# Kernel optimization log

Hardware: AMD Instinct MI355X
Metric: run time of the kernel (lower is better)

## Reference

```python
import jax, jax.numpy as jnp
import numpy as np

B, N, K, DEG = 512, 128, 8, 16
NR = 200            # num_rels (padding idx = NR)
INP, SEM, EMB, L = 32, 16, 32, 3
FEAT = INP - SEM
NN = B * N
E = NN * DEG
OUT = L * EMB       # 96


def _gru_cell(x, h, Wih, Whh, bih, bhh):
    gi = x @ Wih.T + bih
    gh = h @ Whh.T + bhh
    ir, iz, i_n = jnp.split(gi, 3, axis=-1)
    hr, hz, hn = jnp.split(gh, 3, axis=-1)
    r = jax.nn.sigmoid(ir + hr)
    z = jax.nn.sigmoid(iz + hz)
    n = jnp.tanh(i_n + r * hn)
    return (1.0 - z) * n + z * h


def _run_gru(xs, h0, Wih, Whh, bih, bhh):
    # xs: [T, batch, in]
    def step(h, x):
        h2 = _gru_cell(x, h, Wih, Whh, bih, bhh)
        return h2, h2
    hT, ys = jax.lax.scan(step, h0, xs)
    return ys, hT


def _forward(feat, out_nei_rels, in_nei_rels, r_label_node, src, dst, etype, rel_labels,
             rel_emb, w_rel2ent_W, w_rel2ent_b, W_msg, W_self, b_gnn, W_rel,
             gru_bias, gru_Wih_f, gru_Whh_f, gru_bih_f, gru_bhh_f,
             gru_Wih_b, gru_Whh_b, gru_bih_b, gru_bhh_b,
             Wo_W, Wo_b, path_Wih, path_Whh, path_bih, path_bhh, fc_W, fc_b):
    # --- init_ent_emb_matrix: neighbor-relation attention vs target relation ---
    out_e = rel_emb[out_nei_rels]                      # [NN,K,INP]
    in_e = rel_emb[in_nei_rels]                        # [NN,K,INP]
    tgt = rel_emb[r_label_node]                        # [NN,INP]
    out_att = jax.nn.softmax(jnp.einsum('nkd,nd->nk', out_e, tgt), axis=1)
    in_att = jax.nn.softmax(jnp.einsum('nkd,nd->nk', in_e, tgt), axis=1)
    out_sem = jnp.einsum('nk,nkd->nd', out_att, out_e)
    in_sem = jnp.einsum('nk,nkd->nd', in_att, in_e)
    sem = jax.nn.sigmoid(jnp.concatenate([out_sem, in_sem], axis=1) @ w_rel2ent_W + w_rel2ent_b)
    h = jnp.concatenate([feat, sem], axis=1)           # [NN,INP]

    # --- RGCN-style relational message passing; repr = concat of layer outputs ---
    r = rel_emb
    deg = jnp.maximum(jax.ops.segment_sum(jnp.ones((E,), h.dtype), dst, NN), 1.0)[:, None]
    reprs = []
    for l in range(L):
        msg = h[src] * r[etype]                        # [E,EMB]  (gather-heavy)
        agg = jax.ops.segment_sum(msg, dst, NN) / deg  # mean aggregation
        h = jax.nn.relu(agg @ W_msg[l] + h @ W_self[l] + b_gnn[l])
        r = r @ W_rel[l]                               # relation stream (padding row stays 0)
        reprs.append(h)
    repr_ = jnp.concatenate(reprs, axis=1)             # [NN,OUT]
    r_emb_out = r                                      # [NR+1,EMB]

    # --- BatchGRU: bidirectional GRU over each graph's node sequence ---
    node = repr_.reshape(B, N, OUT)
    message = jax.nn.relu(node + gru_bias)
    h0 = jnp.max(node, axis=1)                         # per-graph max init hidden
    xs = jnp.swapaxes(message, 0, 1)                   # [N,B,OUT]
    ys_f, _ = _run_gru(xs, h0, gru_Wih_f, gru_Whh_f, gru_bih_f, gru_bhh_f)
    ys_b, _ = _run_gru(xs[::-1], h0, gru_Wih_b, gru_Whh_b, gru_bih_b, gru_bhh_b)
    gru_out = jnp.concatenate([ys_f, ys_b[::-1]], axis=-1)  # [N,B,2*OUT]
    repr2 = jax.nn.relu(jnp.swapaxes(gru_out, 0, 1).reshape(NN, 2 * OUT))
    node_hidden = jax.nn.relu(repr2 @ Wo_W + Wo_b)     # [NN,OUT]

    nh = node_hidden.reshape(B, N, OUT)
    g_out = jnp.mean(nh, axis=1)                       # mean_nodes
    head_embs = nh[:, 0]                               # node id==1 is node 0 of each graph
    tail_embs = nh[:, 1]                               # node id==2 is node 1 of each graph

    # --- nei_rel_path: GRU over (h_r, r_t, t_r) triples, attention aggregation ---
    in_rels = in_nei_rels.reshape(B, N, K)
    heads_rels = in_rels[:, 0]                         # [B,K]
    tails_rels = in_rels[:, 1]                         # [B,K]
    P = K * K
    paths = jnp.stack([
        jnp.repeat(heads_rels, K, axis=1),
        jnp.broadcast_to(rel_labels[:, None], (B, P)),
        jnp.tile(tails_rels, (1, K)),
    ], axis=-1).reshape(B * P, 3)
    pe = r_emb_out[paths]                              # [B*P,3,EMB]
    _, last = _run_gru(jnp.swapaxes(pe, 0, 1), jnp.zeros((B * P, EMB), pe.dtype),
                       path_Wih, path_Whh, path_bih, path_bhh)
    last = last.reshape(B, P, EMB)
    r_lab_e = r_emb_out[rel_labels]                    # [B,EMB]
    atts = jax.nn.softmax(jnp.einsum('bpe,be->bp', last, r_lab_e), axis=1)
    g_p = jnp.einsum('bp,bpe->be', atts, last)         # [B,EMB]

    g_rep = jnp.concatenate([g_out, head_embs, tail_embs, r_lab_e, g_p], axis=1)  # [B,352]
    return g_rep @ fc_W + fc_b                         # [B,1]


def setup_inputs():
    key = jax.random.key(0)
    ks = jax.random.split(key, 40)
    idx = iter(range(40))
    def nk():
        return ks[next(idx)]
    def _p(shape, scale=0.1):
        return jax.random.normal(nk(), shape, jnp.float32) * scale

    feat = jax.random.normal(nk(), (NN, FEAT), jnp.float32)
    out_nei_rels = jax.random.randint(nk(), (NN, K), 0, NR)
    in_nei_rels = jax.random.randint(nk(), (NN, K), 0, NR)
    rel_labels = jax.random.randint(nk(), (B,), 0, NR)
    r_label_node = jnp.repeat(rel_labels, N)
    gid = jnp.arange(E) // (N * DEG)                   # edges stay within their graph
    src = gid * N + jax.random.randint(nk(), (E,), 0, N)
    dst = gid * N + jax.random.randint(nk(), (E,), 0, N)
    etype = jax.random.randint(nk(), (E,), 0, NR)
    rel_emb = jax.random.normal(nk(), (NR + 1, INP), jnp.float32) * 0.5
    rel_emb = rel_emb.at[NR].set(0.0)                  # padding_idx row

    return {
        'feat': feat, 'out_nei_rels': out_nei_rels, 'in_nei_rels': in_nei_rels,
        'r_label_node': r_label_node, 'src': src, 'dst': dst, 'etype': etype,
        'rel_labels': rel_labels, 'rel_emb': rel_emb,
        'w_rel2ent_W': _p((2 * INP, SEM)), 'w_rel2ent_b': _p((SEM,)),
        'W_msg': _p((L, EMB, EMB)), 'W_self': _p((L, EMB, EMB)),
        'b_gnn': _p((L, EMB)), 'W_rel': _p((L, INP, INP)),
        'gru_bias': _p((OUT,)),
        'gru_Wih_f': _p((3 * OUT, OUT)), 'gru_Whh_f': _p((3 * OUT, OUT)),
        'gru_bih_f': _p((3 * OUT,)), 'gru_bhh_f': _p((3 * OUT,)),
        'gru_Wih_b': _p((3 * OUT, OUT)), 'gru_Whh_b': _p((3 * OUT, OUT)),
        'gru_bih_b': _p((3 * OUT,)), 'gru_bhh_b': _p((3 * OUT,)),
        'Wo_W': _p((2 * OUT, OUT)), 'Wo_b': _p((OUT,)),
        'path_Wih': _p((3 * EMB, EMB)), 'path_Whh': _p((3 * EMB, EMB)),
        'path_bih': _p((3 * EMB,)), 'path_bhh': _p((3 * EMB,)),
        'fc_W': _p((3 * OUT + 2 * EMB, 1)), 'fc_b': _p((1,)),
    }


def reference(feat, out_nei_rels, in_nei_rels, r_label_node, src, dst, etype, rel_labels,
              rel_emb, w_rel2ent_W, w_rel2ent_b, W_msg, W_self, b_gnn, W_rel,
              gru_bias, gru_Wih_f, gru_Whh_f, gru_bih_f, gru_bhh_f,
              gru_Wih_b, gru_Whh_b, gru_bih_b, gru_bhh_b,
              Wo_W, Wo_b, path_Wih, path_Whh, path_bih, path_bhh, fc_W, fc_b):
    return _forward(feat, out_nei_rels, in_nei_rels, r_label_node, src, dst, etype, rel_labels,
                    rel_emb, w_rel2ent_W, w_rel2ent_b, W_msg, W_self, b_gnn, W_rel,
                    gru_bias, gru_Wih_f, gru_Whh_f, gru_bih_f, gru_bhh_f,
                    gru_Wih_b, gru_Whh_b, gru_bih_b, gru_bhh_b,
                    Wo_W, Wo_b, path_Wih, path_Whh, path_bih, path_bhh, fc_W, fc_b)
```

## Files before the change

kernel.cpp:

```cpp
#include <hip/hip_runtime.h>
#include <math.h>

#define BB 512
#define NT 128
#define NREL 201
#define NNODE (BB*NT)
#define NEDGE (NNODE*16)

typedef float f32x4 __attribute__((ext_vector_type(4)));

__device__ __forceinline__ float sigm(float x) { return 1.f/(1.f + __expf(-x)); }

__global__ __launch_bounds__(96) void k_rel2(const float* __restrict__ rel_emb,
                                             const float* __restrict__ W_rel,
                                             const float* __restrict__ pWih,
                                             const float* __restrict__ pbih,
                                             float* __restrict__ r123,
                                             float* __restrict__ XI) {
  __shared__ float ra[32], rb[32];
  int r = blockIdx.x, tid = threadIdx.x;
  if (tid < 32) ra[tid] = rel_emb[r*32 + tid];
  __syncthreads();
  if (tid < 32) {
    float s = 0.f;
    #pragma unroll
    for (int d = 0; d < 32; ++d) s += ra[d]*W_rel[d*32 + tid];
    rb[tid] = s; r123[0*NREL*32 + r*32 + tid] = s;
  }
  __syncthreads();
  if (tid < 32) {
    float s = 0.f;
    #pragma unroll
    for (int d = 0; d < 32; ++d) s += rb[d]*W_rel[1024 + d*32 + tid];
    ra[tid] = s; r123[1*NREL*32 + r*32 + tid] = s;
  }
  __syncthreads();
  if (tid < 32) {
    float s = 0.f;
    #pragma unroll
    for (int d = 0; d < 32; ++d) s += ra[d]*W_rel[2048 + d*32 + tid];
    rb[tid] = s; r123[2*NREL*32 + r*32 + tid] = s;
  }
  __syncthreads();
  float s = pbih[tid];
  #pragma unroll
  for (int d = 0; d < 32; ++d) s += rb[d]*pWih[tid*32 + d];
  XI[r*96 + tid] = s;
}

__global__ __launch_bounds__(256) void k_wt1(const float* __restrict__ Wih_f,
                                             const float* __restrict__ Wih_b,
                                             const float* __restrict__ bih_f,
                                             const float* __restrict__ bih_b,
                                             float* __restrict__ WT1,
                                             float* __restrict__ bcat) {
  int i = blockIdx.x*256 + threadIdx.x;
  if (i < 96*576) {
    int k = i / 576, j = i - k*576;
    WT1[i] = (j < 288) ? Wih_f[j*96 + k] : Wih_b[(j-288)*96 + k];
  }
  if (i < 576) bcat[i] = (i < 288) ? bih_f[i] : bih_b[i-288];
}

__device__ __forceinline__ void sem_att(const float* __restrict__ rel_emb,
                                        const int rels[8], const float tgt[32],
                                        float out[32]) {
  float dots[8]; float mx = -1e30f;
  #pragma unroll
  for (int k = 0; k < 8; ++k) {
    const float4* er = (const float4*)(rel_emb + rels[k]*32);
    float s = 0.f;
    #pragma unroll
    for (int q = 0; q < 8; ++q) {
      float4 v = er[q];
      s += v.x*tgt[4*q+0] + v.y*tgt[4*q+1] + v.z*tgt[4*q+2] + v.w*tgt[4*q+3];
    }
    dots[k] = s; mx = fmaxf(mx, s);
  }
  float den = 0.f;
  #pragma unroll
  for (int k = 0; k < 8; ++k) { float e = __expf(dots[k]-mx); dots[k] = e; den += e; }
  float inv = 1.f/den;
  #pragma unroll
  for (int d = 0; d < 32; ++d) out[d] = 0.f;
  #pragma unroll
  for (int k = 0; k < 8; ++k) {
    const float4* er = (const float4*)(rel_emb + rels[k]*32);
    float a = dots[k]*inv;
    #pragma unroll
    for (int q = 0; q < 8; ++q) {
      float4 v = er[q];
      out[4*q+0] += a*v.x; out[4*q+1] += a*v.y; out[4*q+2] += a*v.z; out[4*q+3] += a*v.w;
    }
  }
}

__global__ __launch_bounds__(256) void k_sem(
    const float* __restrict__ feat, const int* __restrict__ out_rels,
    const int* __restrict__ in_rels, const int* __restrict__ r_label_node,
    const float* __restrict__ rel_emb, const float* __restrict__ W,
    const float* __restrict__ bias, float* __restrict__ hin) {
  int n = blockIdx.x*256 + threadIdx.x;
  float tgt[32];
  {
    const float4* tr = (const float4*)(rel_emb + r_label_node[n]*32);
    #pragma unroll
    for (int q = 0; q < 8; ++q) {
      float4 v = tr[q];
      tgt[4*q+0]=v.x; tgt[4*q+1]=v.y; tgt[4*q+2]=v.z; tgt[4*q+3]=v.w;
    }
  }
  int ro[8], ri[8];
  #pragma unroll
  for (int k = 0; k < 8; ++k) { ro[k] = out_rels[n*8+k]; ri[k] = in_rels[n*8+k]; }
  float osem[32], isem[32];
  sem_att(rel_emb, ro, tgt, osem);
  sem_att(rel_emb, ri, tgt, isem);
  const float4* fr = (const float4*)(feat + (size_t)n*16);
  float4* ho = (float4*)(hin + (size_t)n*32);
  #pragma unroll
  for (int q = 0; q < 4; ++q) ho[q] = fr[q];
  #pragma unroll
  for (int j = 0; j < 16; ++j) {
    float s = bias[j];
    #pragma unroll
    for (int d = 0; d < 32; ++d) s += osem[d]*W[d*16+j] + isem[d]*W[(32+d)*16+j];
    hin[(size_t)n*32 + 16 + j] = sigm(s);
  }
}

__global__ __launch_bounds__(512) void k_gnn3(
    const float* __restrict__ hin, const float* __restrict__ rel_emb,
    const float* __restrict__ r123,
    const int* __restrict__ src, const int* __restrict__ dst, const int* __restrict__ etype,
    const float* __restrict__ W_msg, const float* __restrict__ W_self,
    const float* __restrict__ b_gnn,
    float* __restrict__ AT, float* __restrict__ ghid0) {
  __shared__ __align__(16) float hl[NT*36];
  __shared__ __align__(16) float hnew[NT*33];
  __shared__ float rl[NREL*32];
  __shared__ unsigned short eidx[2048];
  __shared__ float scratch[16][32];
  __shared__ int cnt[128], fill[128], scanv[128], rowstart[129];
  int g = blockIdx.x;
  int tid = threadIdx.x;
  int d = tid & 31, grp = tid >> 5;

  for (int i = tid; i < NT*32; i += 512) {
    int row = i >> 5, col = i & 31;
    hl[row*36 + col] = hin[(size_t)(g*NT + row)*32 + col];
  }
  if (tid < 128) { cnt[tid] = 0; fill[tid] = 0; }
  __syncthreads();
  for (int i = tid; i < 2048; i += 512)
    atomicAdd(&cnt[dst[g*2048 + i] - g*NT], 1);
  __syncthreads();
  if (tid < 128) scanv[tid] = cnt[tid];
  __syncthreads();
  #pragma unroll
  for (int off = 1; off < 128; off <<= 1) {
    int v = 0;
    if (tid < 128 && tid >= off) v = scanv[tid - off];
    __syncthreads();
    if (tid < 128) scanv[tid] += v;
    __syncthreads();
  }
  if (tid < 128) { rowstart[tid+1] = scanv[tid]; if (tid == 0) rowstart[0] = 0; }
  __syncthreads();
  for (int i = tid; i < 2048; i += 512) {
    int e = g*2048 + i;
    int dl = dst[e] - g*NT;
    int slot = rowstart[dl] + atomicAdd(&fill[dl], 1);
    eidx[slot] = (unsigned short)(((src[e] - g*NT) << 8) | etype[e]);
  }

  for (int l = 0; l < 3; ++l) {
    const float* rsrc = (l == 0) ? rel_emb : (r123 + (size_t)(l-1)*NREL*32);
    for (int i = tid; i < NREL*32; i += 512) rl[i] = rsrc[i];
    float wm[32], ws[32];
    #pragma unroll
    for (int dd = 0; dd < 32; ++dd) {
      wm[dd] = W_msg[l*1024 + dd*32 + d];
      ws[dd] = W_self[l*1024 + dd*32 + d];
    }
    float bj = b_gnn[l*32 + d];
    __syncthreads();
    for (int k2 = 0; k2 < 8; ++k2) {
      int n = grp + k2*16;
      int e0 = rowstart[n], e1 = rowstart[n+1];
      float acc = 0.f;
      for (int e = e0; e < e1; ++e) {
        int pk = eidx[e];
        acc += hl[(pk >> 8)*36 + d] * rl[(pk & 255)*32 + d];
      }
      scratch[grp][d] = acc;
      float invd = 1.f / (float)((e1 - e0) > 0 ? (e1 - e0) : 1);
      float sa = 0.f, sh = 0.f;
      #pragma unroll
      for (int dd = 0; dd < 32; ++dd) {
        sa += scratch[grp][dd]*wm[dd];
        sh += hl[n*36 + dd]*ws[dd];
      }
      hnew[n*33 + d] = fmaxf(bj + invd*sa + sh, 0.f);
    }
    __syncthreads();
    for (int i = tid; i < NT*32; i += 512) {
      int row = i >> 5, col = i & 31;
      hl[row*36 + col] = hnew[row*33 + col];
    }
    #pragma unroll
    for (int pass = 0; pass < 8; ++pass) {
      int col = (pass << 2) + (tid >> 7);
      int row = tid & 127;
      AT[(size_t)(l*32 + col)*NNODE + g*NT + row] = hnew[row*33 + col];
    }
    {
      float m = -1e30f;
      #pragma unroll
      for (int k2 = 0; k2 < 8; ++k2) m = fmaxf(m, hnew[(grp + k2*16)*33 + d]);
      scratch[grp][d] = m;
    }
    __syncthreads();
    if (tid < 32) {
      float m = -1e30f;
      #pragma unroll
      for (int p2 = 0; p2 < 16; ++p2) m = fmaxf(m, scratch[p2][tid]);
      ghid0[g*96 + l*32 + tid] = m;
    }
    __syncthreads();
  }
}

__global__ __launch_bounds__(256) void k_gemm1(
    const float* __restrict__ AT, const float* __restrict__ gbias,
    const float* __restrict__ WT1, const float* __restrict__ bcat,
    float* __restrict__ GI) {
  __shared__ __align__(16) float As[96*128];
  __shared__ __align__(16) float Bs[96*64];
  int mb = blockIdx.x;
  int m0 = mb*128;
  int tid = threadIdx.x;
  for (int i = tid; i < 3072; i += 256) {
    int r = i >> 5, c4 = i & 31;
    float4 v = *(const float4*)&AT[(size_t)r*NNODE + m0 + c4*4];
    float b = gbias[r];
    float4 o = make_float4(fmaxf(v.x+b,0.f), fmaxf(v.y+b,0.f), fmaxf(v.z+b,0.f), fmaxf(v.w+b,0.f));
    *(float4*)&As[r*128 + c4*4] = o;
  }
  int tc = tid & 15, tr = tid >> 4;
  int r0 = tr*8, c0 = tc*4;
  for (int nb = 0; nb < 9; ++nb) {
    int n0 = nb*64;
    for (int i = tid; i < 1536; i += 256) {
      int r = i >> 4, c4 = i & 15;
      *(float4*)&Bs[r*64 + c4*4] = *(const float4*)&WT1[r*576 + n0 + c4*4];
    }
    __syncthreads();
    float acc[8][4] = {};
    #pragma unroll 4
    for (int k = 0; k < 96; ++k) {
      float4 a0 = *(float4*)&As[k*128 + r0];
      float4 a1 = *(float4*)&As[k*128 + r0 + 4];
      float4 b  = *(float4*)&Bs[k*64 + c0];
      acc[0][0]+=a0.x*b.x; acc[0][1]+=a0.x*b.y; acc[0][2]+=a0.x*b.z; acc[0][3]+=a0.x*b.w;
      acc[1][0]+=a0.y*b.x; acc[1][1]+=a0.y*b.y; acc[1][2]+=a0.y*b.z; acc[1][3]+=a0.y*b.w;
      acc[2][0]+=a0.z*b.x; acc[2][1]+=a0.z*b.y; acc[2][2]+=a0.z*b.z; acc[2][3]+=a0.z*b.w;
      acc[3][0]+=a0.w*b.x; acc[3][1]+=a0.w*b.y; acc[3][2]+=a0.w*b.z; acc[3][3]+=a0.w*b.w;
      acc[4][0]+=a1.x*b.x; acc[4][1]+=a1.x*b.y; acc[4][2]+=a1.x*b.z; acc[4][3]+=a1.x*b.w;
      acc[5][0]+=a1.y*b.x; acc[5][1]+=a1.y*b.y; acc[5][2]+=a1.y*b.z; acc[5][3]+=a1.y*b.w;
      acc[6][0]+=a1.z*b.x; acc[6][1]+=a1.z*b.y; acc[6][2]+=a1.z*b.z; acc[6][3]+=a1.z*b.w;
      acc[7][0]+=a1.w*b.x; acc[7][1]+=a1.w*b.y; acc[7][2]+=a1.w*b.z; acc[7][3]+=a1.w*b.w;
    }
    float4 bia = *(const float4*)&bcat[n0 + c0];
    #pragma unroll
    for (int r = 0; r < 8; ++r) {
      f32x4 o = { acc[r][0]+bia.x, acc[r][1]+bia.y, acc[r][2]+bia.z, acc[r][3]+bia.w };
      __builtin_nontemporal_store(o, (f32x4*)&GI[(size_t)(m0 + r0 + r)*576 + n0 + c0]);
    }
    __syncthreads();
  }
}

#define PIN4(v) asm volatile("" : "+v"(v.x), "+v"(v.y), "+v"(v.z), "+v"(v.w))
#define DOT16(acc, W0,W1,W2,W3, X0,X1,X2,X3) \
  acc += W0.x*X0.x + W0.y*X0.y + W0.z*X0.z + W0.w*X0.w \
       + W1.x*X1.x + W1.y*X1.y + W1.z*X1.z + W1.w*X1.w \
       + W2.x*X2.x + W2.y*X2.y + W2.z*X2.z + W2.w*X2.w \
       + W3.x*X3.x + W3.y*X3.y + W3.z*X3.z + W3.w*X3.w

__global__ __launch_bounds__(576, 1) void k_gru(
    const float* __restrict__ Whh_f, const float* __restrict__ bhh_f,
    const float* __restrict__ Whh_b, const float* __restrict__ bhh_b,
    const float* __restrict__ GI, const float* __restrict__ ghid0,
    float* __restrict__ AT2) {
  __shared__ __align__(16) float h_lds[4][96];
  __shared__ float part[4][288][9];
  int bx = blockIdx.x;
  int dir = bx >> 7;
  int gbase = (bx & 127) * 4;
  int tid = threadIdx.x;
  int c = tid % 96;
  int p = tid / 96;
  bool fin = (tid < 384);
  int s = p;

  const float* Whh = dir ? Whh_b : Whh_f;
  const float4* wr0 = (const float4*)(Whh + (size_t)c*96 + p*16);
  const float4* wr1 = (const float4*)(Whh + (size_t)(96+c)*96 + p*16);
  const float4* wr2 = (const float4*)(Whh + (size_t)(192+c)*96 + p*16);
  float4 wa0=wr0[0], wa1=wr0[1], wa2=wr0[2], wa3=wr0[3];
  float4 wb0=wr1[0], wb1=wr1[1], wb2=wr1[2], wb3=wr1[3];
  float4 wc0=wr2[0], wc1=wr2[1], wc2=wr2[2], wc3=wr2[3];

  float bh0=0.f, bh1=0.f, bh2=0.f;
  float gi0=0.f, gi1=0.f, gi2=0.f;
  if (fin) {
    const float* bhh = dir ? bhh_b : bhh_f;
    bh0 = bhh[c]; bh1 = bhh[96+c]; bh2 = bhh[192+c];
    h_lds[s][c] = ghid0[(gbase+s)*96 + c];
    int pos0 = dir ? 127 : 0;
    const float* g = GI + (size_t)((gbase+s)*128 + pos0)*576 + dir*288;
    gi0 = g[c]; gi1 = g[96+c]; gi2 = g[192+c];
  }
  __syncthreads();
  for (int t = 0; t < 128; ++t) {
    PIN4(wa0); PIN4(wa1); PIN4(wa2); PIN4(wa3);
    PIN4(wb0); PIN4(wb1); PIN4(wb2); PIN4(wb3);
    PIN4(wc0); PIN4(wc1); PIN4(wc2); PIN4(wc3);
    int pos = dir ? (127-t) : t;
    float gn0=0.f, gn1=0.f, gn2=0.f;
    if (fin && t < 127) {
      int posn = dir ? (126-t) : (t+1);
      const float* g = GI + (size_t)((gbase+s)*128 + posn)*576 + dir*288;
      gn0 = g[c]; gn1 = g[96+c]; gn2 = g[192+c];
    }
    #pragma unroll
    for (int s4 = 0; s4 < 4; ++s4) {
      const float4* hh = (const float4*)&h_lds[s4][p*16];
      float4 x0=hh[0], x1=hh[1], x2=hh[2], x3=hh[3];
      float q0=0.f, q1=0.f, q2=0.f;
      DOT16(q0, wa0,wa1,wa2,wa3, x0,x1,x2,x3);
      DOT16(q1, wb0,wb1,wb2,wb3, x0,x1,x2,x3);
      DOT16(q2, wc0,wc1,wc2,wc3, x0,x1,x2,x3);
      part[s4][c][p]     = q0;
      part[s4][96+c][p]  = q1;
      part[s4][192+c][p] = q2;
    }
    __syncthreads();
    if (fin) {
      const float* pr = part[s][c];
      const float* pz = part[s][96+c];
      const float* pn = part[s][192+c];
      float ghr = pr[0]+pr[1]+pr[2]+pr[3]+pr[4]+pr[5] + bh0;
      float ghz = pz[0]+pz[1]+pz[2]+pz[3]+pz[4]+pz[5] + bh1;
      float ghn = pn[0]+pn[1]+pn[2]+pn[3]+pn[4]+pn[5] + bh2;
      float r  = sigm(gi0 + ghr);
      float z  = sigm(gi1 + ghz);
      float nn = tanhf(gi2 + r*ghn);
      float hv = (1.f - z)*nn + z*h_lds[s][c];
      h_lds[s][c] = hv;
      AT2[(size_t)(dir*96 + c)*NNODE + (gbase+s)*128 + pos] = fmaxf(hv, 0.f);
      gi0 = gn0; gi1 = gn1; gi2 = gn2;
    }
    __syncthreads();
  }
}

__global__ __launch_bounds__(384) void k_gemm2p(
    const float* __restrict__ AT2, const float* __restrict__ WoW,
    const float* __restrict__ Wob, float* __restrict__ goutb,
    float* __restrict__ headb, float* __restrict__ tailb) {
  __shared__ __align__(16) float As[96*64];
  __shared__ __align__(16) float Bs[96*96];
  __shared__ float red[16][100];
  int m0 = blockIdx.x*64;
  int g = m0 >> 7;
  int tid = threadIdx.x;
  int tc = tid % 24, tr = tid / 24;
  int r0 = tr*4, c0 = tc*4;
  float acc[4][4] = {};
  for (int kc = 0; kc < 2; ++kc) {
    for (int i = tid; i < 1536; i += 384) {
      int r = i >> 4, c4 = i & 15;
      *(float4*)&As[r*64 + c4*4] = *(const float4*)&AT2[(size_t)(kc*96 + r)*NNODE + m0 + c4*4];
    }
    for (int i = tid; i < 2304; i += 384) {
      int r = i / 24, c4 = i % 24;
      *(float4*)&Bs[r*96 + c4*4] = *(const float4*)&WoW[(size_t)(kc*96 + r)*96 + c4*4];
    }
    __syncthreads();
    #pragma unroll 8
    for (int k = 0; k < 96; ++k) {
      float4 a = *(float4*)&As[k*64 + r0];
      float4 b = *(float4*)&Bs[k*96 + c0];
      acc[0][0] += a.x*b.x; acc[0][1] += a.x*b.y; acc[0][2] += a.x*b.z; acc[0][3] += a.x*b.w;
      acc[1][0] += a.y*b.x; acc[1][1] += a.y*b.y; acc[1][2] += a.y*b.z; acc[1][3] += a.y*b.w;
      acc[2][0] += a.z*b.x; acc[2][1] += a.z*b.y; acc[2][2] += a.z*b.z; acc[2][3] += a.z*b.w;
      acc[3][0] += a.w*b.x; acc[3][1] += a.w*b.y; acc[3][2] += a.w*b.z; acc[3][3] += a.w*b.w;
    }
    __syncthreads();
  }
  float4 bia = *(const float4*)&Wob[c0];
  float nv[4][4];
  #pragma unroll
  for (int r = 0; r < 4; ++r) {
    nv[r][0] = fmaxf(acc[r][0]+bia.x, 0.f);
    nv[r][1] = fmaxf(acc[r][1]+bia.y, 0.f);
    nv[r][2] = fmaxf(acc[r][2]+bia.z, 0.f);
    nv[r][3] = fmaxf(acc[r][3]+bia.w, 0.f);
  }
  #pragma unroll
  for (int cj = 0; cj < 4; ++cj)
    red[tr][c0+cj] = nv[0][cj] + nv[1][cj] + nv[2][cj] + nv[3][cj];
  if ((m0 & 127) == 0 && tr == 0) {
    #pragma unroll
    for (int cj = 0; cj < 4; ++cj) {
      headb[g*96 + c0 + cj] = nv[0][cj];
      tailb[g*96 + c0 + cj] = nv[1][cj];
    }
  }
  __syncthreads();
  if (tid < 96) {
    float s = 0.f;
    #pragma unroll
    for (int t2 = 0; t2 < 16; ++t2) s += red[t2][tid];
    atomicAdd(&goutb[g*96 + tid], s);
  }
}

__global__ __launch_bounds__(128) void k_path(
    const float* __restrict__ XI, const int* __restrict__ in_rels,
    const int* __restrict__ labels, const float* __restrict__ pWhh,
    const float* __restrict__ pbhh, float* __restrict__ last) {
  __shared__ __align__(16) float wsh[96*32];
  __shared__ float bsh[96];
  __shared__ float hbuf[128*33];
  int tid = threadIdx.x;
  for (int i = tid; i < 96*32; i += 128) wsh[i] = pWhh[i];
  if (tid < 96) bsh[tid] = pbhh[tid];
  int p = blockIdx.x*128 + tid;
  int b = p >> 6, pp = p & 63;
  int rid0 = in_rels[b*1024 + (pp >> 3)];
  int rid1 = labels[b];
  int rid2 = in_rels[b*1024 + 8 + (pp & 7)];
  __syncthreads();
  float* hs = &hbuf[tid*33];
  {
    const float* xi = XI + rid0*96;
    #pragma unroll
    for (int gg = 0; gg < 32; ++gg) {
      float r = sigm(xi[gg] + bsh[gg]);
      float z = sigm(xi[32+gg] + bsh[32+gg]);
      float nn = tanhf(xi[64+gg] + r*bsh[64+gg]);
      hs[gg] = (1.f - z)*nn;
    }
  }
  float4 h4[8];
  #pragma unroll
  for (int q = 0; q < 8; ++q) h4[q] = make_float4(hs[4*q], hs[4*q+1], hs[4*q+2], hs[4*q+3]);
  for (int s = 0; s < 2; ++s) {
    const float* xi = XI + (s == 0 ? rid1 : rid2)*96;
    for (int gg = 0; gg < 32; ++gg) {
      float ar = bsh[gg], az = bsh[32+gg], an = bsh[64+gg];
      const float4* wr = (const float4*)&wsh[gg*32];
      const float4* wz = (const float4*)&wsh[(32+gg)*32];
      const float4* wn = (const float4*)&wsh[(64+gg)*32];
      #pragma unroll
      for (int q = 0; q < 8; ++q) {
        float4 hv = h4[q]; float4 w;
        w = wr[q]; ar += hv.x*w.x + hv.y*w.y + hv.z*w.z + hv.w*w.w;
        w = wz[q]; az += hv.x*w.x + hv.y*w.y + hv.z*w.z + hv.w*w.w;
        w = wn[q]; an += hv.x*w.x + hv.y*w.y + hv.z*w.z + hv.w*w.w;
      }
      float r = sigm(xi[gg] + ar);
      float z = sigm(xi[32+gg] + az);
      float nn = tanhf(xi[64+gg] + r*an);
      hs[gg] = (1.f - z)*nn + z*hs[gg];
    }
    #pragma unroll
    for (int q = 0; q < 8; ++q) h4[q] = make_float4(hs[4*q], hs[4*q+1], hs[4*q+2], hs[4*q+3]);
  }
  float* lp = last + (size_t)p*32;
  #pragma unroll
  for (int d = 0; d < 32; ++d) lp[d] = hs[d];
}

__global__ __launch_bounds__(64) void k_final(
    const float* __restrict__ last, const float* __restrict__ r3,
    const int* __restrict__ labels, const float* __restrict__ goutb,
    const float* __restrict__ headb, const float* __restrict__ tailb,
    const float* __restrict__ fcW, const float* __restrict__ fcb,
    float* __restrict__ out) {
  __shared__ float red[64*33];
  __shared__ float gpl[32];
  int b = blockIdx.x, lane = threadIdx.x;
  const float* rl = r3 + labels[b]*32;
  float l32[32];
  {
    const float4* lr = (const float4*)(last + (size_t)(b*64 + lane)*32);
    #pragma unroll
    for (int q = 0; q < 8; ++q) {
      float4 v = lr[q];
      l32[4*q+0]=v.x; l32[4*q+1]=v.y; l32[4*q+2]=v.z; l32[4*q+3]=v.w;
    }
  }
  float s = 0.f;
  #pragma unroll
  for (int d = 0; d < 32; ++d) s += l32[d]*rl[d];
  float mx = s;
  #pragma unroll
  for (int off = 32; off > 0; off >>= 1) mx = fmaxf(mx, __shfl_xor(mx, off));
  float e = __expf(s - mx);
  float den = e;
  #pragma unroll
  for (int off = 32; off > 0; off >>= 1) den += __shfl_xor(den, off);
  float att = e / den;
  #pragma unroll
  for (int d = 0; d < 32; ++d) red[lane*33 + d] = att*l32[d];
  __syncthreads();
  if (lane < 32) {
    float gp = 0.f;
    for (int p2 = 0; p2 < 64; ++p2) gp += red[p2*33 + lane];
    gpl[lane] = gp;
  }
  __syncthreads();
  float acc = 0.f;
  for (int i = lane; i < 352; i += 64) {
    float v;
    if (i < 96)       v = goutb[b*96 + i] * 0.0078125f;
    else if (i < 192) v = headb[b*96 + (i-96)];
    else if (i < 288) v = tailb[b*96 + (i-192)];
    else if (i < 320) v = rl[i-288];
    else              v = gpl[i-320];
    acc += v*fcW[i];
  }
  #pragma unroll
  for (int off = 32; off > 0; off >>= 1) acc += __shfl_xor(acc, off);
  if (lane == 0) out[b] = acc + fcb[0];
}

extern "C" void kernel_launch(void* const* d_in, const int* in_sizes, int n_in,
                              void* d_out, int out_size, void* d_ws, size_t ws_size,
                              hipStream_t stream) {
  const float* feat       = (const float*)d_in[0];
  const int*   out_rels   = (const int*)d_in[1];
  const int*   in_rels    = (const int*)d_in[2];
  const int*   r_label_nd = (const int*)d_in[3];
  const int*   src        = (const int*)d_in[4];
  const int*   dst        = (const int*)d_in[5];
  const int*   etype      = (const int*)d_in[6];
  const int*   rel_labels = (const int*)d_in[7];
  const float* rel_emb    = (const float*)d_in[8];
  const float* w2e_W      = (const float*)d_in[9];
  const float* w2e_b      = (const float*)d_in[10];
  const float* W_msg      = (const float*)d_in[11];
  const float* W_self     = (const float*)d_in[12];
  const float* b_gnn      = (const float*)d_in[13];
  const float* W_rel      = (const float*)d_in[14];
  const float* gru_bias   = (const float*)d_in[15];
  const float* Wih_f      = (const float*)d_in[16];
  const float* Whh_f      = (const float*)d_in[17];
  const float* bih_f      = (const float*)d_in[18];
  const float* bhh_f      = (const float*)d_in[19];
  const float* Wih_b      = (const float*)d_in[20];
  const float* Whh_b      = (const float*)d_in[21];
  const float* bih_b      = (const float*)d_in[22];
  const float* bhh_b      = (const float*)d_in[23];
  const float* Wo_W       = (const float*)d_in[24];
  const float* Wo_b       = (const float*)d_in[25];
  const float* pWih       = (const float*)d_in[26];
  const float* pWhh       = (const float*)d_in[27];
  const float* pbih       = (const float*)d_in[28];
  const float* pbhh       = (const float*)d_in[29];
  const float* fcW        = (const float*)d_in[30];
  const float* fcb        = (const float*)d_in[31];
  float* out = (float*)d_out;

  float* p = (float*)d_ws;
  float* hin   = p; p += (size_t)NNODE*32;
  float* R1    = p; p += (size_t)NNODE*192;
  float* AT    = R1;
  float* AT2   = R1;
  float* R2    = p; p += (size_t)NNODE*576;
  float* GI    = R2;
  float* r123  = p; p += 3*NREL*32;
  float* WT1   = p; p += 96*576;
  float* bcat  = p; p += 576;
  float* XI    = p; p += NREL*96;
  float* ghid0 = p; p += BB*96;
  float* goutb = p; p += BB*96;
  float* headb = p; p += BB*96;
  float* tailb = p; p += BB*96;
  float* lastb = p; p += (size_t)BB*64*32;

  hipMemsetAsync(goutb, 0, BB*96*sizeof(float), stream);
  k_rel2<<<NREL, 96, 0, stream>>>(rel_emb, W_rel, pWih, pbih, r123, XI);
  k_wt1<<<(96*576+255)/256, 256, 0, stream>>>(Wih_f, Wih_b, bih_f, bih_b, WT1, bcat);
  k_sem<<<NNODE/256, 256, 0, stream>>>(feat, out_rels, in_rels, r_label_nd,
                                       rel_emb, w2e_W, w2e_b, hin);
  k_gnn3<<<BB, 512, 0, stream>>>(hin, rel_emb, r123, src, dst, etype,
                                 W_msg, W_self, b_gnn, AT, ghid0);
  k_gemm1<<<512, 256, 0, stream>>>(AT, gru_bias, WT1, bcat, GI);
  k_gru<<<256, 576, 0, stream>>>(Whh_f, bhh_f, Whh_b, bhh_b, GI, ghid0, AT2);
  k_gemm2p<<<1024, 384, 0, stream>>>(AT2, Wo_W, Wo_b, goutb, headb, tailb);
  k_path<<<256, 128, 0, stream>>>(XI, in_rels, rel_labels, pWhh, pbhh, lastb);
  k_final<<<BB, 64, 0, stream>>>(lastb, r123 + 2*NREL*32, rel_labels,
                                 goutb, headb, tailb, fcW, fcb, out);
}
```

Measured before the change: 533.9 us.

## Restructure GRU recurrence to reduce partial sums via wave shuffles with double-buffered hidden state

The recurrent GRU kernel drops from 576 to 384 threads. Each group of 4 adjacent lanes now splits the 96-wide hidden dot product into 24-element chunks and combines the partial sums with xor shuffles, replacing the shared-memory partial-sum array and its extra barrier. The hidden state is double-buffered in LDS and kept in a register, so each timestep needs one barrier instead of two. The cost is more weight registers per thread (72 floats) and fewer threads sharing the per-step dot-product work.

```diff
diff --git a/kernel.cpp b/kernel.cpp
--- a/kernel.cpp
+++ b/kernel.cpp
@@ -282,87 +282,85 @@
 }
 
 #define PIN4(v) asm volatile("" : "+v"(v.x), "+v"(v.y), "+v"(v.z), "+v"(v.w))
-#define DOT16(acc, W0,W1,W2,W3, X0,X1,X2,X3) \
+#define DOT24(acc, W0,W1,W2,W3,W4,W5, X0,X1,X2,X3,X4,X5) \
   acc += W0.x*X0.x + W0.y*X0.y + W0.z*X0.z + W0.w*X0.w \
        + W1.x*X1.x + W1.y*X1.y + W1.z*X1.z + W1.w*X1.w \
        + W2.x*X2.x + W2.y*X2.y + W2.z*X2.z + W2.w*X2.w \
-       + W3.x*X3.x + W3.y*X3.y + W3.z*X3.z + W3.w*X3.w
-
-__global__ __launch_bounds__(576, 1) void k_gru(
+       + W3.x*X3.x + W3.y*X3.y + W3.z*X3.z + W3.w*X3.w \
+       + W4.x*X4.x + W4.y*X4.y + W4.z*X4.z + W4.w*X4.w \
+       + W5.x*X5.x + W5.y*X5.y + W5.z*X5.z + W5.w*X5.w
+
+__global__ __launch_bounds__(384, 1) void k_gru(
     const float* __restrict__ Whh_f, const float* __restrict__ bhh_f,
     const float* __restrict__ Whh_b, const float* __restrict__ bhh_b,
     const float* __restrict__ GI, const float* __restrict__ ghid0,
     float* __restrict__ AT2) {
-  __shared__ __align__(16) float h_lds[4][96];
-  __shared__ float part[4][288][9];
+  __shared__ __align__(16) float h_lds[2][4][100];
   int bx = blockIdx.x;
   int dir = bx >> 7;
   int gbase = (bx & 127) * 4;
   int tid = threadIdx.x;
-  int c = tid % 96;
-  int p = tid / 96;
-  bool fin = (tid < 384);
-  int s = p;
+  int c = tid >> 2;
+  int p = tid & 3;
 
   const float* Whh = dir ? Whh_b : Whh_f;
-  const float4* wr0 = (const float4*)(Whh + (size_t)c*96 + p*16);
-  const float4* wr1 = (const float4*)(Whh + (size_t)(96+c)*96 + p*16);
-  const float4* wr2 = (const float4*)(Whh + (size_t)(192+c)*96 + p*16);
-  float4 wa0=wr0[0], wa1=wr0[1], wa2=wr0[2], wa3=wr0[3];
-  float4 wb0=wr1[0], wb1=wr1[1], wb2=wr1[2], wb3=wr1[3];
-  float4 wc0=wr2[0], wc1=wr2[1], wc2=wr2[2], wc3=wr2[3];
-
-  float bh0=0.f, bh1=0.f, bh2=0.f;
-  float gi0=0.f, gi1=0.f, gi2=0.f;
-  if (fin) {
-    const float* bhh = dir ? bhh_b : bhh_f;
-    bh0 = bhh[c]; bh1 = bhh[96+c]; bh2 = bhh[192+c];
-    h_lds[s][c] = ghid0[(gbase+s)*96 + c];
-    int pos0 = dir ? 127 : 0;
-    const float* g = GI + (size_t)((gbase+s)*128 + pos0)*576 + dir*288;
-    gi0 = g[c]; gi1 = g[96+c]; gi2 = g[192+c];
-  }
-  __syncthreads();
+  const float* bhh = dir ? bhh_b : bhh_f;
+  const float4* wr0 = (const float4*)(Whh + (size_t)c*96 + p*24);
+  const float4* wr1 = (const float4*)(Whh + (size_t)(96+c)*96 + p*24);
+  const float4* wr2 = (const float4*)(Whh + (size_t)(192+c)*96 + p*24);
+  float4 wa0=wr0[0], wa1=wr0[1], wa2=wr0[2], wa3=wr0[3], wa4=wr0[4], wa5=wr0[5];
+  float4 wb0=wr1[0], wb1=wr1[1], wb2=wr1[2], wb3=wr1[3], wb4=wr1[4], wb5=wr1[5];
+  float4 wc0=wr2[0], wc1=wr2[1], wc2=wr2[2], wc3=wr2[3], wc4=wr2[4], wc5=wr2[5];
+
+  float bh0 = bhh[c], bh1 = bhh[96+c], bh2 = bhh[192+c];
+  float hreg = ghid0[(gbase+p)*96 + c];
+  h_lds[0][p][c] = hreg;
+  int pos0 = dir ? 127 : 0;
+  const float* g0 = GI + (size_t)((gbase+p)*128 + pos0)*576 + dir*288;
+  float gi0 = g0[c], gi1 = g0[96+c], gi2 = g0[192+c];
+  __syncthreads();
+  int cur = 0;
   for (int t = 0; t < 128; ++t) {
-    PIN4(wa0); PIN4(wa1); PIN4(wa2); PIN4(wa3);
-    PIN4(wb0); PIN4(wb1); PIN4(wb2); PIN4(wb3);
-    PIN4(wc0); PIN4(wc1); PIN4(wc2); PIN4(wc3);
+    PIN4(wa0); PIN4(wa1); PIN4(wa2); PIN4(wa3); PIN4(wa4); PIN4(wa5);
+    PIN4(wb0); PIN4(wb1); PIN4(wb2); PIN4(wb3); PIN4(wb4); PIN4(wb5);
+    PIN4(wc0); PIN4(wc1); PIN4(wc2); PIN4(wc3); PIN4(wc4); PIN4(wc5);
     int pos = dir ? (127-t) : t;
     float gn0=0.f, gn1=0.f, gn2=0.f;
-    if (fin && t < 127) {
+    if (t < 127) {
       int posn = dir ? (126-t) : (t+1);
-      const float* g = GI + (size_t)((gbase+s)*128 + posn)*576 + dir*288;
+      const float* g = GI + (size_t)((gbase+p)*128 + posn)*576 + dir*288;
       gn0 = g[c]; gn1 = g[96+c]; gn2 = g[192+c];
     }
+    float pr[4], pz[4], pn[4];
     #pragma unroll
     for (int s4 = 0; s4 < 4; ++s4) {
-      const float4* hh = (const float4*)&h_lds[s4][p*16];
-      float4 x0=hh[0], x1=hh[1], x2=hh[2], x3=hh[3];
+      const float4* hh = (const float4*)&h_lds[cur][s4][p*24];
+      float4 x0=hh[0], x1=hh[1], x2=hh[2], x3=hh[3], x4=hh[4], x5=hh[5];
       float q0=0.f, q1=0.f, q2=0.f;
-      DOT16(q0, wa0,wa1,wa2,wa3, x0,x1,x2,x3);
-      DOT16(q1, wb0,wb1,wb2,wb3, x0,x1,x2,x3);
-      DOT16(q2, wc0,wc1,wc2,wc3, x0,x1,x2,x3);
-      part[s4][c][p]     = q0;
-      part[s4][96+c][p]  = q1;
-      part[s4][192+c][p] = q2;
-    }
-    __syncthreads();
-    if (fin) {
-      const float* pr = part[s][c];
-      const float* pz = part[s][96+c];
-      const float* pn = part[s][192+c];
-      float ghr = pr[0]+pr[1]+pr[2]+pr[3]+pr[4]+pr[5] + bh0;
-      float ghz = pz[0]+pz[1]+pz[2]+pz[3]+pz[4]+pz[5] + bh1;
-      float ghn = pn[0]+pn[1]+pn[2]+pn[3]+pn[4]+pn[5] + bh2;
-      float r  = sigm(gi0 + ghr);
-      float z  = sigm(gi1 + ghz);
-      float nn = tanhf(gi2 + r*ghn);
-      float hv = (1.f - z)*nn + z*h_lds[s][c];
-      h_lds[s][c] = hv;
-      AT2[(size_t)(dir*96 + c)*NNODE + (gbase+s)*128 + pos] = fmaxf(hv, 0.f);
-      gi0 = gn0; gi1 = gn1; gi2 = gn2;
-    }
-    __syncthreads();
+      DOT24(q0, wa0,wa1,wa2,wa3,wa4,wa5, x0,x1,x2,x3,x4,x5);
+      DOT24(q1, wb0,wb1,wb2,wb3,wb4,wb5, x0,x1,x2,x3,x4,x5);
+      DOT24(q2, wc0,wc1,wc2,wc3,wc4,wc5, x0,x1,x2,x3,x4,x5);
+      pr[s4]=q0; pz[s4]=q1; pn[s4]=q2;
+    }
+    #pragma unroll
+    for (int s4 = 0; s4 < 4; ++s4) {
+      pr[s4] += __shfl_xor(pr[s4], 1); pr[s4] += __shfl_xor(pr[s4], 2);
+      pz[s4] += __shfl_xor(pz[s4], 1); pz[s4] += __shfl_xor(pz[s4], 2);
+      pn[s4] += __shfl_xor(pn[s4], 1); pn[s4] += __shfl_xor(pn[s4], 2);
+    }
+    float ghr = (p==0)?pr[0]:(p==1)?pr[1]:(p==2)?pr[2]:pr[3];
+    float ghz = (p==0)?pz[0]:(p==1)?pz[1]:(p==2)?pz[2]:pz[3];
+    float ghn = (p==0)?pn[0]:(p==1)?pn[1]:(p==2)?pn[2]:pn[3];
+    float r  = sigm(gi0 + ghr + bh0);
+    float z  = sigm(gi1 + ghz + bh1);
+    float nn = tanhf(gi2 + r*(ghn + bh2));
+    float hv = (1.f - z)*nn + z*hreg;
+    hreg = hv;
+    h_lds[cur^1][p][c] = hv;
+    AT2[(size_t)(dir*96 + c)*NNODE + (gbase+p)*128 + pos] = fmaxf(hv, 0.f);
+    gi0 = gn0; gi1 = gn1; gi2 = gn2;
+    __syncthreads();
+    cur ^= 1;
   }
 }
 
@@ -601,7 +599,7 @@
   k_gnn3<<<BB, 512, 0, stream>>>(hin, rel_emb, r123, src, dst, etype,
                                  W_msg, W_self, b_gnn, AT, ghid0);
   k_gemm1<<<512, 256, 0, stream>>>(AT, gru_bias, WT1, bcat, GI);
-  k_gru<<<256, 576, 0, stream>>>(Whh_f, bhh_f, Whh_b, bhh_b, GI, ghid0, AT2);
+  k_gru<<<256, 384, 0, stream>>>(Whh_f, bhh_f, Whh_b, bhh_b, GI, ghid0, AT2);
   k_gemm2p<<<1024, 384, 0, stream>>>(AT2, Wo_W, Wo_b, goutb, headb, tailb);
   k_path<<<256, 128, 0, stream>>>(XI, in_rels, rel_labels, pWhh, pbhh, lastb);
   k_final<<<BB, 64, 0, stream>>>(lastb, r123 + 2*NREL*32, rel_labels,
```

Result: slower. 629.3 us (+17.9%).

## Use bf16 MFMA for the GRU input projection GEMM

Applied to the files above, without the earlier changes.

Rewrites the GRU input-projection GEMM to run on bf16 MFMA instructions instead of scalar fp32 FMAs. The activations are converted to bf16 into LDS in transposed layout, and the weights are pre-converted to bf16 in their natural row-major layout. B fragments are read directly from global memory and A fragments are kept in registers across all column blocks. This cuts ALU work and LDS traffic, at the cost of bf16 rounding of the inputs, which may change numerical accuracy.

```diff
diff --git a/kernel.cpp b/kernel.cpp
--- a/kernel.cpp
+++ b/kernel.cpp
@@ -8,8 +8,15 @@
 #define NEDGE (NNODE*16)
 
 typedef float f32x4 __attribute__((ext_vector_type(4)));
+typedef __attribute__((ext_vector_type(8))) short bf16x8;
 
 __device__ __forceinline__ float sigm(float x) { return 1.f/(1.f + __expf(-x)); }
+
+__device__ __forceinline__ unsigned short f2bf(float f) {
+  unsigned u; __builtin_memcpy(&u, &f, 4);
+  unsigned r = u + 0x7fffu + ((u >> 16) & 1u);
+  return (unsigned short)(r >> 16);
+}
 
 __global__ __launch_bounds__(96) void k_rel2(const float* __restrict__ rel_emb,
                                              const float* __restrict__ W_rel,
@@ -52,12 +59,13 @@
                                              const float* __restrict__ Wih_b,
                                              const float* __restrict__ bih_f,
                                              const float* __restrict__ bih_b,
-                                             float* __restrict__ WT1,
+                                             unsigned short* __restrict__ WT1bt,
                                              float* __restrict__ bcat) {
   int i = blockIdx.x*256 + threadIdx.x;
-  if (i < 96*576) {
-    int k = i / 576, j = i - k*576;
-    WT1[i] = (j < 288) ? Wih_f[j*96 + k] : Wih_b[(j-288)*96 + k];
+  if (i < 576*96) {
+    int j = i / 96;
+    float v = (j < 288) ? Wih_f[i] : Wih_b[i - 288*96];
+    WT1bt[i] = f2bf(v);
   }
   if (i < 576) bcat[i] = (i < 288) ? bih_f[i] : bih_b[i-288];
 }
@@ -231,53 +239,55 @@
   }
 }
 
-__global__ __launch_bounds__(256) void k_gemm1(
+__global__ __launch_bounds__(256) void k_gemm1m(
     const float* __restrict__ AT, const float* __restrict__ gbias,
-    const float* __restrict__ WT1, const float* __restrict__ bcat,
+    const unsigned short* __restrict__ WT1bt, const float* __restrict__ bcat,
     float* __restrict__ GI) {
-  __shared__ __align__(16) float As[96*128];
-  __shared__ __align__(16) float Bs[96*64];
-  int mb = blockIdx.x;
-  int m0 = mb*128;
+  __shared__ unsigned short As[128*104];
+  int m0 = blockIdx.x * 128;
   int tid = threadIdx.x;
-  for (int i = tid; i < 3072; i += 256) {
+  for (int i = tid; i < 96*32; i += 256) {
     int r = i >> 5, c4 = i & 31;
     float4 v = *(const float4*)&AT[(size_t)r*NNODE + m0 + c4*4];
     float b = gbias[r];
-    float4 o = make_float4(fmaxf(v.x+b,0.f), fmaxf(v.y+b,0.f), fmaxf(v.z+b,0.f), fmaxf(v.w+b,0.f));
-    *(float4*)&As[r*128 + c4*4] = o;
-  }
-  int tc = tid & 15, tr = tid >> 4;
-  int r0 = tr*8, c0 = tc*4;
+    float o0 = fmaxf(v.x+b,0.f), o1 = fmaxf(v.y+b,0.f);
+    float o2 = fmaxf(v.z+b,0.f), o3 = fmaxf(v.w+b,0.f);
+    As[(c4*4+0)*104 + r] = f2bf(o0);
+    As[(c4*4+1)*104 + r] = f2bf(o1);
+    As[(c4*4+2)*104 + r] = f2bf(o2);
+    As[(c4*4+3)*104 + r] = f2bf(o3);
+  }
+  __syncthreads();
+  int w = tid >> 6, l = tid & 63;
+  int lr = l & 15, lh = l >> 4;
+  bf16x8 afr[2][3];
+  #pragma unroll
+  for (int tm = 0; tm < 2; ++tm)
+    #pragma unroll
+    for (int kc = 0; kc < 3; ++kc)
+      afr[tm][kc] = *(const bf16x8*)&As[((w*2+tm)*16 + lr)*104 + kc*32 + lh*8];
   for (int nb = 0; nb < 9; ++nb) {
     int n0 = nb*64;
-    for (int i = tid; i < 1536; i += 256) {
-      int r = i >> 4, c4 = i & 15;
-      *(float4*)&Bs[r*64 + c4*4] = *(const float4*)&WT1[r*576 + n0 + c4*4];
-    }
-    __syncthreads();
-    float acc[8][4] = {};
-    #pragma unroll 4
-    for (int k = 0; k < 96; ++k) {
-      float4 a0 = *(float4*)&As[k*128 + r0];
-      float4 a1 = *(float4*)&As[k*128 + r0 + 4];
-      float4 b  = *(float4*)&Bs[k*64 + c0];
-      acc[0][0]+=a0.x*b.x; acc[0][1]+=a0.x*b.y; acc[0][2]+=a0.x*b.z; acc[0][3]+=a0.x*b.w;
-      acc[1][0]+=a0.y*b.x; acc[1][1]+=a0.y*b.y; acc[1][2]+=a0.y*b.z; acc[1][3]+=a0.y*b.w;
-      acc[2][0]+=a0.z*b.x; acc[2][1]+=a0.z*b.y; acc[2][2]+=a0.z*b.z; acc[2][3]+=a0.z*b.w;
-      acc[3][0]+=a0.w*b.x; acc[3][1]+=a0.w*b.y; acc[3][2]+=a0.w*b.z; acc[3][3]+=a0.w*b.w;
-      acc[4][0]+=a1.x*b.x; acc[4][1]+=a1.x*b.y; acc[4][2]+=a1.x*b.z; acc[4][3]+=a1.x*b.w;
-      acc[5][0]+=a1.y*b.x; acc[5][1]+=a1.y*b.y; acc[5][2]+=a1.y*b.z; acc[5][3]+=a1.y*b.w;
-      acc[6][0]+=a1.z*b.x; acc[6][1]+=a1.z*b.y; acc[6][2]+=a1.z*b.z; acc[6][3]+=a1.z*b.w;
-      acc[7][0]+=a1.w*b.x; acc[7][1]+=a1.w*b.y; acc[7][2]+=a1.w*b.z; acc[7][3]+=a1.w*b.w;
-    }
-    float4 bia = *(const float4*)&bcat[n0 + c0];
-    #pragma unroll
-    for (int r = 0; r < 8; ++r) {
-      f32x4 o = { acc[r][0]+bia.x, acc[r][1]+bia.y, acc[r][2]+bia.z, acc[r][3]+bia.w };
-      __builtin_nontemporal_store(o, (f32x4*)&GI[(size_t)(m0 + r0 + r)*576 + n0 + c0]);
-    }
-    __syncthreads();
+    #pragma unroll
+    for (int tn = 0; tn < 4; ++tn) {
+      int col = n0 + tn*16 + lr;
+      const unsigned short* bp = WT1bt + (size_t)col*96 + lh*8;
+      bf16x8 b0 = *(const bf16x8*)(bp);
+      bf16x8 b1 = *(const bf16x8*)(bp + 32);
+      bf16x8 b2 = *(const bf16x8*)(bp + 64);
+      float bb = bcat[col];
+      #pragma unroll
+      for (int tm = 0; tm < 2; ++tm) {
+        f32x4 acc = {bb, bb, bb, bb};
+        acc = __builtin_amdgcn_mfma_f32_16x16x32_bf16(afr[tm][0], b0, acc, 0, 0, 0);
+        acc = __builtin_amdgcn_mfma_f32_16x16x32_bf16(afr[tm][1], b1, acc, 0, 0, 0);
+        acc = __builtin_amdgcn_mfma_f32_16x16x32_bf16(afr[tm][2], b2, acc, 0, 0, 0);
+        int rbase = m0 + (w*2+tm)*16 + lh*4;
+        #pragma unroll
+        for (int r = 0; r < 4; ++r)
+          __builtin_nontemporal_store(acc[r], &GI[(size_t)(rbase + r)*576 + col]);
+      }
+    }
   }
 }
 
@@ -584,7 +594,7 @@
   float* R2    = p; p += (size_t)NNODE*576;
   float* GI    = R2;
   float* r123  = p; p += 3*NREL*32;
-  float* WT1   = p; p += 96*576;
+  unsigned short* WT1bt = (unsigned short*)p; p += (576*96)/2;
   float* bcat  = p; p += 576;
   float* XI    = p; p += NREL*96;
   float* ghid0 = p; p += BB*96;
@@ -595,12 +605,12 @@
 
   hipMemsetAsync(goutb, 0, BB*96*sizeof(float), stream);
   k_rel2<<<NREL, 96, 0, stream>>>(rel_emb, W_rel, pWih, pbih, r123, XI);
-  k_wt1<<<(96*576+255)/256, 256, 0, stream>>>(Wih_f, Wih_b, bih_f, bih_b, WT1, bcat);
+  k_wt1<<<(576*96+255)/256, 256, 0, stream>>>(Wih_f, Wih_b, bih_f, bih_b, WT1bt, bcat);
   k_sem<<<NNODE/256, 256, 0, stream>>>(feat, out_rels, in_rels, r_label_nd,
                                        rel_emb, w2e_W, w2e_b, hin);
   k_gnn3<<<BB, 512, 0, stream>>>(hin, rel_emb, r123, src, dst, etype,
                                  W_msg, W_self, b_gnn, AT, ghid0);
-  k_gemm1<<<512, 256, 0, stream>>>(AT, gru_bias, WT1, bcat, GI);
+  k_gemm1m<<<512, 256, 0, stream>>>(AT, gru_bias, WT1bt, bcat, GI);
   k_gru<<<256, 576, 0, stream>>>(Whh_f, bhh_f, Whh_b, bhh_b, GI, ghid0, AT2);
   k_gemm2p<<<1024, 384, 0, stream>>>(AT2, Wo_W, Wo_b, goutb, headb, tailb);
   k_path<<<256, 128, 0, stream>>>(XI, in_rels, rel_labels, pWhh, pbhh, lastb);
```

New measurement: 504.0 us. -5.6%, faster.
